# Optimization experiments

Hardware: AMD Instinct MI355X
Metric: run time of the kernel (lower is better)

## Reference

```python
import jax, jax.numpy as jnp
import numpy as np

B, N, F_IN, F_OUT, E = 8, 4096, 256, 256, 131072


def setup_inputs() -> dict:
    key = jax.random.key(0)
    kx, ke, kw = jax.random.split(key, 3)
    x = jax.random.normal(kx, (B, N, F_IN), dtype=jnp.float32)
    edge_index = jax.random.randint(ke, (2, E), 0, N, dtype=jnp.int32)
    # Xavier-uniform init for weight, zeros for bias (matches reset_parameters)
    limit = float(np.sqrt(6.0 / (F_IN + F_OUT)))
    weight = jax.random.uniform(kw, (F_IN, F_OUT), dtype=jnp.float32,
                                minval=-limit, maxval=limit)
    bias = jnp.zeros((F_OUT,), dtype=jnp.float32)
    return {"x": x, "edge_index": edge_index, "weight": weight, "bias": bias}


def reference(x, edge_index, weight, bias):
    # x: (B, N, F_in) -> transformed: (B, N, F_out)
    xt = jnp.einsum("bnf,fo->bno", x, weight)
    n_nodes = x.shape[1]
    # Adjacency is identical for every batch element in the original
    # (built from the same edge_index inside the loop) -> build once.
    # .set(1.0) matches torch's `adj[src, dst] = 1.0` (duplicates collapse).
    adj = jnp.zeros((n_nodes, n_nodes), dtype=xt.dtype)
    adj = adj.at[edge_index[0], edge_index[1]].set(1.0)
    degree = adj.sum(axis=1, keepdims=True) + 1e-6  # (N, 1)
    adj_norm = adj / degree
    # Aggregate: out[b] = adj_norm @ xt[b], batched as one einsum
    out = jnp.einsum("ij,bjf->bif", adj_norm, xt)
    return out + bias
```

## Files before the change

kernel.cpp:

```cpp
#include <hip/hip_runtime.h>
#include <hip/hip_bf16.h>


#define GC_B     8
#define GC_N     4096
#define GC_F     256
#define GC_E     131072
#define GC_M     (GC_B * GC_N)
#define MASK_WPR (GC_N / 32)

typedef __attribute__((ext_vector_type(8))) short         short8;
typedef __attribute__((ext_vector_type(4))) float         float4v;
typedef __attribute__((ext_vector_type(4))) unsigned int  uint4v;

static __device__ __forceinline__ unsigned short f2bf_rne(float f) {
    unsigned u = __builtin_bit_cast(unsigned, f);
    u += 0x7fffu + ((u >> 16) & 1u);
    return (unsigned short)(u >> 16);
}
static __device__ __forceinline__ float bflo(unsigned u) {
    return __builtin_bit_cast(float, u << 16);
}
static __device__ __forceinline__ float bfhi(unsigned u) {
    return __builtin_bit_cast(float, u & 0xffff0000u);
}

__global__ void build_mask_kernel(const int* __restrict__ ei,
                                  unsigned* __restrict__ mask) {
    int e = blockIdx.x * blockDim.x + threadIdx.x;
    if (e < GC_E) {
        int s = ei[e];
        int d = ei[GC_E + e];
        atomicOr(&mask[s * MASK_WPR + (d >> 5)], 1u << (d & 31));
    }
}

__global__ __launch_bounds__(128) void pack_mask_kernel(unsigned* __restrict__ mask) {
    __shared__ unsigned short list[256];
    __shared__ int cnt;
    const int i = blockIdx.x;
    const int t = threadIdx.x;

    if (t == 0) cnt = 0;
    unsigned w = mask[i * MASK_WPR + t];
    __syncthreads();

    const int base = t * 32;
    while (w) {
        const int b = __builtin_ctz(w);
        w &= w - 1;
        const int p = atomicAdd(&cnt, 1);
        if (p < 255) list[p + 1] = (unsigned short)(base + b);
    }
    __syncthreads();
    if (t == 0) list[0] = (unsigned short)(cnt < 255 ? cnt : 255);
    __syncthreads();

    ((unsigned*)(mask + i * MASK_WPR))[t] = ((const unsigned*)list)[t];
}

__global__ __launch_bounds__(256) void convert_x_kernel(
        const float* __restrict__ X, unsigned short* __restrict__ Xb) {
    const size_t i = ((size_t)blockIdx.x * 256 + threadIdx.x) * 8;
    const float4v v0 = *(const float4v*)(X + i);
    const float4v v1 = *(const float4v*)(X + i + 4);
    union { unsigned short h[8]; short8 s; } u;
    u.h[0] = f2bf_rne(v0[0]); u.h[1] = f2bf_rne(v0[1]);
    u.h[2] = f2bf_rne(v0[2]); u.h[3] = f2bf_rne(v0[3]);
    u.h[4] = f2bf_rne(v1[0]); u.h[5] = f2bf_rne(v1[1]);
    u.h[6] = f2bf_rne(v1[2]); u.h[7] = f2bf_rne(v1[3]);
    *(short8*)(Xb + i) = u.s;
}

__global__ __launch_bounds__(256) void aggregate_kernel(
        const unsigned short* __restrict__ Xb, const unsigned* __restrict__ mask,
        unsigned short* __restrict__ aggb) {
    __shared__ unsigned short list[4][256];

    const int w    = threadIdx.x >> 6;
    const int lane = threadIdx.x & 63;
    const int b    = blockIdx.x & 7;
    const int i    = (blockIdx.x >> 3) * 4 + w;
    const int bn   = b * GC_N + i;

    if (lane < 32)
        ((uint4v*)list[w])[lane] = ((const uint4v*)(mask + i * MASK_WPR))[lane];
    __syncthreads();

    const int deg = list[w][0];
    const int fg  = lane & 31;
    const int ks  = lane >> 5;

    const unsigned short* xbase = Xb + (size_t)b * GC_N * GC_F + fg * 8;
    float accA[8] = {}, accB[8] = {};
    int k = ks;
    for (; k + 2 < deg; k += 4) {
        const uint4v v0 = *(const uint4v*)(xbase + (size_t)list[w][1 + k] * GC_F);
        const uint4v v1 = *(const uint4v*)(xbase + (size_t)list[w][3 + k] * GC_F);
        #pragma unroll
        for (int e = 0; e < 4; e++) {
            accA[2 * e]     += bflo(v0[e]);
            accA[2 * e + 1] += bfhi(v0[e]);
            accB[2 * e]     += bflo(v1[e]);
            accB[2 * e + 1] += bfhi(v1[e]);
        }
    }
    for (; k < deg; k += 2) {
        const uint4v v0 = *(const uint4v*)(xbase + (size_t)list[w][1 + k] * GC_F);
        #pragma unroll
        for (int e = 0; e < 4; e++) {
            accA[2 * e]     += bflo(v0[e]);
            accA[2 * e + 1] += bfhi(v0[e]);
        }
    }

    float acc[8];
    #pragma unroll
    for (int e = 0; e < 8; e++) {
        acc[e] = accA[e] + accB[e];
        acc[e] += __shfl_xor(acc[e], 32, 64);
    }

    if (ks == 0) {
        const float inv = 1.0f / ((float)deg + 1e-6f);
        uint4v o;
        #pragma unroll
        for (int e = 0; e < 4; e++) {
            const float s0 = acc[2 * e] * inv;
            const float s1 = acc[2 * e + 1] * inv;
            o[e] = (unsigned)f2bf_rne(s0) | ((unsigned)f2bf_rne(s1) << 16);
        }
        *(uint4v*)(aggb + (size_t)bn * GC_F + fg * 8) = o;
    }
}

__global__ __launch_bounds__(256) void convert_w_kernel(
        const float* __restrict__ W, unsigned short* __restrict__ Wt) {
    const int n = blockIdx.x;
    const int k = threadIdx.x;
    Wt[n * GC_F + k] = f2bf_rne(W[k * GC_F + n]);
}

#define MROWS 128
__global__ __launch_bounds__(256) void gemm_bias_kernel(
        const unsigned short* __restrict__ Ab,
        const unsigned short* __restrict__ Wt,
        const float* __restrict__ bias, float* __restrict__ out) {
    const int lane = threadIdx.x & 63;
    const int r    = lane & 15;
    const int q    = lane >> 4;
    const int f0   = blockIdx.y * 64 + 16 * (threadIdx.x >> 6);

    const unsigned short* wp = Wt + (size_t)(f0 + r) * GC_F + q * 8;
    short8 wfr[8];
    #pragma unroll
    for (int kc = 0; kc < 8; kc++) wfr[kc] = *(const short8*)(wp + kc * 32);
    const float4v bv = *(const float4v*)(bias + f0 + 4 * q);

    const int mbase = blockIdx.x * MROWS;
    #pragma unroll 2
    for (int mt = 0; mt < MROWS / 16; mt++) {
        const int m0 = mbase + mt * 16;
        const unsigned short* ap = Ab + (size_t)(m0 + r) * GC_F + q * 8;
        float4v acc = {0, 0, 0, 0};
        #pragma unroll
        for (int kc = 0; kc < 8; kc++)
            acc = __builtin_amdgcn_mfma_f32_16x16x32_bf16(
                wfr[kc], *(const short8*)(ap + kc * 32), acc, 0, 0, 0);
        *(float4v*)(out + (size_t)(m0 + r) * GC_F + f0 + 4 * q) = acc + bv;
    }
}

extern "C" void kernel_launch(void* const* d_in, const int* in_sizes, int n_in,
                              void* d_out, int out_size, void* d_ws, size_t ws_size,
                              hipStream_t stream) {
    const float* x      = (const float*)d_in[0];
    const int*   ei     = (const int*)d_in[1];
    const float* weight = (const float*)d_in[2];
    const float* bias   = (const float*)d_in[3];
    float*       out    = (float*)d_out;

    unsigned short* aggb = (unsigned short*)d_ws;
    unsigned*       mask = (unsigned*)((char*)d_ws + (size_t)GC_M * GC_F * 2);
    unsigned short* Xb   = (unsigned short*)((char*)d_ws + (size_t)GC_M * GC_F * 2
                                             + (size_t)GC_N * MASK_WPR * 4);
    unsigned short* Wt   = Xb;

    hipMemsetAsync(mask, 0, (size_t)GC_N * MASK_WPR * sizeof(unsigned), stream);
    build_mask_kernel<<<(GC_E + 255) / 256, 256, 0, stream>>>(ei, mask);
    pack_mask_kernel<<<GC_N, 128, 0, stream>>>(mask);

    convert_x_kernel<<<(GC_M * GC_F) / 2048, 256, 0, stream>>>(x, Xb);

    aggregate_kernel<<<GC_M / 4, 256, 0, stream>>>(Xb, mask, aggb);

    convert_w_kernel<<<GC_F, GC_F, 0, stream>>>(weight, Wt);

    dim3 ggrid(GC_M / MROWS, GC_F / 64);
    gemm_bias_kernel<<<ggrid, 256, 0, stream>>>(aggb, Wt, bias, out);
}
```

Measured before the change: 161.3 us.

## Fuse prep kernels and build neighbor lists directly via atomics during mask build

Merges the x conversion, weight transpose-conversion, mask zeroing and counter zeroing into one prep kernel, replacing the memset and two launches. The mask build now appends each newly set destination to a per-row list using atomicAdd, which removes the separate pack kernel. The aggregate kernel reads the list and count from fixed-capacity buffers, and accumulation uses float2 vectors. This cuts launches and a pass over the mask, but the list order becomes nondeterministic, degree is capped at 128 entries, and Wt no longer aliases Xb.

```diff
diff --git a/kernel.cpp b/kernel.cpp
--- a/kernel.cpp
+++ b/kernel.cpp
@@ -8,8 +8,10 @@
 #define GC_E     131072
 #define GC_M     (GC_B * GC_N)
 #define MASK_WPR (GC_N / 32)
+#define LIST_CAP 128
 
 typedef __attribute__((ext_vector_type(8))) short         short8;
+typedef __attribute__((ext_vector_type(2))) float         float2v;
 typedef __attribute__((ext_vector_type(4))) float         float4v;
 typedef __attribute__((ext_vector_type(4))) unsigned int  uint4v;
 
@@ -25,57 +27,60 @@
     return __builtin_bit_cast(float, u & 0xffff0000u);
 }
 
-__global__ void build_mask_kernel(const int* __restrict__ ei,
-                                  unsigned* __restrict__ mask) {
-    int e = blockIdx.x * blockDim.x + threadIdx.x;
+__global__ __launch_bounds__(256) void prep_kernel(
+        const float* __restrict__ X, const float* __restrict__ W,
+        unsigned short* __restrict__ Xb, unsigned short* __restrict__ Wt,
+        unsigned* __restrict__ mask, unsigned* __restrict__ cnt) {
+    const int blk = blockIdx.x;
+    const int t   = threadIdx.x;
+    if (blk < 4096) {
+        const size_t i = ((size_t)blk * 256 + t) * 8;
+        const float4v v0 = *(const float4v*)(X + i);
+        const float4v v1 = *(const float4v*)(X + i + 4);
+        union { unsigned short h[8]; short8 s; } u;
+        u.h[0] = f2bf_rne(v0[0]); u.h[1] = f2bf_rne(v0[1]);
+        u.h[2] = f2bf_rne(v0[2]); u.h[3] = f2bf_rne(v0[3]);
+        u.h[4] = f2bf_rne(v1[0]); u.h[5] = f2bf_rne(v1[1]);
+        u.h[6] = f2bf_rne(v1[2]); u.h[7] = f2bf_rne(v1[3]);
+        *(short8*)(Xb + i) = u.s;
+    } else if (blk < 4352) {
+        const int n = blk - 4096;
+        Wt[n * GC_F + t] = f2bf_rne(W[t * GC_F + n]);
+    } else if (blk < 4480) {
+        const size_t base = ((size_t)(blk - 4352) * 256 + t) * 4;
+        const uint4v z = {0, 0, 0, 0};
+        #pragma unroll
+        for (int j = 0; j < 4; j++) ((uint4v*)mask)[base + j] = z;
+    } else {
+        const uint4v z = {0, 0, 0, 0};
+        #pragma unroll
+        for (int j = 0; j < 4; j++) ((uint4v*)cnt)[(size_t)t * 4 + j] = z;
+    }
+}
+
+__global__ void build_list_kernel(const int* __restrict__ ei,
+                                  unsigned* __restrict__ mask,
+                                  unsigned* __restrict__ cnt,
+                                  unsigned short* __restrict__ list) {
+    const int e = blockIdx.x * blockDim.x + threadIdx.x;
     if (e < GC_E) {
-        int s = ei[e];
-        int d = ei[GC_E + e];
-        atomicOr(&mask[s * MASK_WPR + (d >> 5)], 1u << (d & 31));
-    }
-}
-
-__global__ __launch_bounds__(128) void pack_mask_kernel(unsigned* __restrict__ mask) {
-    __shared__ unsigned short list[256];
-    __shared__ int cnt;
-    const int i = blockIdx.x;
-    const int t = threadIdx.x;
-
-    if (t == 0) cnt = 0;
-    unsigned w = mask[i * MASK_WPR + t];
-    __syncthreads();
-
-    const int base = t * 32;
-    while (w) {
-        const int b = __builtin_ctz(w);
-        w &= w - 1;
-        const int p = atomicAdd(&cnt, 1);
-        if (p < 255) list[p + 1] = (unsigned short)(base + b);
-    }
-    __syncthreads();
-    if (t == 0) list[0] = (unsigned short)(cnt < 255 ? cnt : 255);
-    __syncthreads();
-
-    ((unsigned*)(mask + i * MASK_WPR))[t] = ((const unsigned*)list)[t];
-}
-
-__global__ __launch_bounds__(256) void convert_x_kernel(
-        const float* __restrict__ X, unsigned short* __restrict__ Xb) {
-    const size_t i = ((size_t)blockIdx.x * 256 + threadIdx.x) * 8;
-    const float4v v0 = *(const float4v*)(X + i);
-    const float4v v1 = *(const float4v*)(X + i + 4);
-    union { unsigned short h[8]; short8 s; } u;
-    u.h[0] = f2bf_rne(v0[0]); u.h[1] = f2bf_rne(v0[1]);
-    u.h[2] = f2bf_rne(v0[2]); u.h[3] = f2bf_rne(v0[3]);
-    u.h[4] = f2bf_rne(v1[0]); u.h[5] = f2bf_rne(v1[1]);
-    u.h[6] = f2bf_rne(v1[2]); u.h[7] = f2bf_rne(v1[3]);
-    *(short8*)(Xb + i) = u.s;
+        const int s = ei[e];
+        const int d = ei[GC_E + e];
+        const unsigned bit = 1u << (d & 31);
+        const unsigned old = atomicOr(&mask[s * MASK_WPR + (d >> 5)], bit);
+        if (!(old & bit)) {
+            const unsigned p = atomicAdd(&cnt[s], 1u);
+            if (p < LIST_CAP) list[s * LIST_CAP + p] = (unsigned short)d;
+        }
+    }
 }
 
 __global__ __launch_bounds__(256) void aggregate_kernel(
-        const unsigned short* __restrict__ Xb, const unsigned* __restrict__ mask,
+        const unsigned short* __restrict__ Xb, const unsigned* __restrict__ cnt,
+        const unsigned short* __restrict__ list,
         unsigned short* __restrict__ aggb) {
-    __shared__ unsigned short list[4][256];
+    __shared__ unsigned short lst[4][LIST_CAP];
+    __shared__ int degs[4];
 
     const int w    = threadIdx.x >> 6;
     const int lane = threadIdx.x & 63;
@@ -83,43 +88,46 @@
     const int i    = (blockIdx.x >> 3) * 4 + w;
     const int bn   = b * GC_N + i;
 
-    if (lane < 32)
-        ((uint4v*)list[w])[lane] = ((const uint4v*)(mask + i * MASK_WPR))[lane];
+    if (lane < 16)
+        ((uint4v*)lst[w])[lane] = ((const uint4v*)(list + i * LIST_CAP))[lane];
+    if (lane == 0) {
+        const unsigned c = cnt[i];
+        degs[w] = (int)(c < LIST_CAP ? c : LIST_CAP);
+    }
     __syncthreads();
 
-    const int deg = list[w][0];
+    const int deg = degs[w];
     const int fg  = lane & 31;
     const int ks  = lane >> 5;
 
     const unsigned short* xbase = Xb + (size_t)b * GC_N * GC_F + fg * 8;
-    float accA[8] = {}, accB[8] = {};
+    float2v accA[4] = {}, accB[4] = {};
     int k = ks;
     for (; k + 2 < deg; k += 4) {
-        const uint4v v0 = *(const uint4v*)(xbase + (size_t)list[w][1 + k] * GC_F);
-        const uint4v v1 = *(const uint4v*)(xbase + (size_t)list[w][3 + k] * GC_F);
+        const uint4v v0 = *(const uint4v*)(xbase + (size_t)lst[w][k] * GC_F);
+        const uint4v v1 = *(const uint4v*)(xbase + (size_t)lst[w][k + 2] * GC_F);
         #pragma unroll
         for (int e = 0; e < 4; e++) {
-            accA[2 * e]     += bflo(v0[e]);
-            accA[2 * e + 1] += bfhi(v0[e]);
-            accB[2 * e]     += bflo(v1[e]);
-            accB[2 * e + 1] += bfhi(v1[e]);
+            accA[e] += (float2v){bflo(v0[e]), bfhi(v0[e])};
+            accB[e] += (float2v){bflo(v1[e]), bfhi(v1[e])};
         }
     }
     for (; k < deg; k += 2) {
-        const uint4v v0 = *(const uint4v*)(xbase + (size_t)list[w][1 + k] * GC_F);
-        #pragma unroll
-        for (int e = 0; e < 4; e++) {
-            accA[2 * e]     += bflo(v0[e]);
-            accA[2 * e + 1] += bfhi(v0[e]);
-        }
+        const uint4v v0 = *(const uint4v*)(xbase + (size_t)lst[w][k] * GC_F);
+        #pragma unroll
+        for (int e = 0; e < 4; e++)
+            accA[e] += (float2v){bflo(v0[e]), bfhi(v0[e])};
     }
 
     float acc[8];
     #pragma unroll
-    for (int e = 0; e < 8; e++) {
-        acc[e] = accA[e] + accB[e];
+    for (int e = 0; e < 4; e++) {
+        acc[2 * e]     = accA[e].x + accB[e].x;
+        acc[2 * e + 1] = accA[e].y + accB[e].y;
+    }
+    #pragma unroll
+    for (int e = 0; e < 8; e++)
         acc[e] += __shfl_xor(acc[e], 32, 64);
-    }
 
     if (ks == 0) {
         const float inv = 1.0f / ((float)deg + 1e-6f);
@@ -132,13 +140,6 @@
         }
         *(uint4v*)(aggb + (size_t)bn * GC_F + fg * 8) = o;
     }
-}
-
-__global__ __launch_bounds__(256) void convert_w_kernel(
-        const float* __restrict__ W, unsigned short* __restrict__ Wt) {
-    const int n = blockIdx.x;
-    const int k = threadIdx.x;
-    Wt[n * GC_F + k] = f2bf_rne(W[k * GC_F + n]);
 }
 
 #define MROWS 128
@@ -180,21 +181,19 @@
     const float* bias   = (const float*)d_in[3];
     float*       out    = (float*)d_out;
 
-    unsigned short* aggb = (unsigned short*)d_ws;
-    unsigned*       mask = (unsigned*)((char*)d_ws + (size_t)GC_M * GC_F * 2);
-    unsigned short* Xb   = (unsigned short*)((char*)d_ws + (size_t)GC_M * GC_F * 2
-                                             + (size_t)GC_N * MASK_WPR * 4);
-    unsigned short* Wt   = Xb;
-
-    hipMemsetAsync(mask, 0, (size_t)GC_N * MASK_WPR * sizeof(unsigned), stream);
-    build_mask_kernel<<<(GC_E + 255) / 256, 256, 0, stream>>>(ei, mask);
-    pack_mask_kernel<<<GC_N, 128, 0, stream>>>(mask);
-
-    convert_x_kernel<<<(GC_M * GC_F) / 2048, 256, 0, stream>>>(x, Xb);
-
-    aggregate_kernel<<<GC_M / 4, 256, 0, stream>>>(Xb, mask, aggb);
-
-    convert_w_kernel<<<GC_F, GC_F, 0, stream>>>(weight, Wt);
+    char* p = (char*)d_ws;
+    unsigned short* aggb = (unsigned short*)p;             p += (size_t)GC_M * GC_F * 2;
+    unsigned short* Xb   = (unsigned short*)p;             p += (size_t)GC_M * GC_F * 2;
+    unsigned short* Wt   = (unsigned short*)p;             p += (size_t)GC_F * GC_F * 2;
+    unsigned*       mask = (unsigned*)p;                   p += (size_t)GC_N * MASK_WPR * 4;
+    unsigned*       cnt  = (unsigned*)p;                   p += (size_t)GC_N * 4;
+    unsigned short* list = (unsigned short*)p;
+
+    prep_kernel<<<4481, 256, 0, stream>>>(x, weight, Xb, Wt, mask, cnt);
+
+    build_list_kernel<<<(GC_E + 255) / 256, 256, 0, stream>>>(ei, mask, cnt, list);
+
+    aggregate_kernel<<<GC_M / 4, 256, 0, stream>>>(Xb, cnt, list, aggb);
 
     dim3 ggrid(GC_M / MROWS, GC_F / 64);
     gemm_bias_kernel<<<ggrid, 256, 0, stream>>>(aggb, Wt, bias, out);
```

Result: slower. 166.4 us (+3.2%).
